# Kernel optimization log

Measured on AMD Instinct MI355X. Metric: run time of the kernel, lower is better.

Reference implementation:

```python
import jax, jax.numpy as jnp
import numpy as np

D_MODEL, D_K, D_V, H = 64, 32, 32, 8
B, HH, WW = 2, 48, 48
NQ = HH * WW


def setup_inputs() -> dict:
    key = jax.random.key(0)
    ks = jax.random.split(key, 16)
    inp = {
        "queries": jax.random.normal(ks[0], (B, D_MODEL, HH, WW), jnp.float32),
        "keys": jax.random.normal(ks[1], (B, D_MODEL, HH, WW), jnp.float32),
        "values": jax.random.normal(ks[2], (B, D_MODEL, HH, WW), jnp.float32),
        "attention_weights": jax.random.uniform(ks[3], (B, H, NQ, NQ), jnp.float32),
        "attention_mask": jax.random.randint(ks[4], (B, H, NQ, NQ), 0, 2) > 0,
        # Linear params: torch init normal(std=0.001) weights, zero bias
        "Wq": 0.001 * jax.random.normal(ks[5], (H * D_K, D_MODEL), jnp.float32),
        "bq": jnp.zeros((H * D_K,), jnp.float32),
        "Wk": 0.001 * jax.random.normal(ks[6], (H * D_K, D_MODEL), jnp.float32),
        "bk": jnp.zeros((H * D_K,), jnp.float32),
        "Wv": 0.001 * jax.random.normal(ks[7], (H * D_V, D_MODEL), jnp.float32),
        "bv": jnp.zeros((H * D_V,), jnp.float32),
        "Wo": 0.001 * jax.random.normal(ks[8], (D_MODEL, H * D_V), jnp.float32),
        "bo": jnp.zeros((D_MODEL,), jnp.float32),
    }
    return inp


def reference(queries, keys, values, attention_weights, attention_mask,
              Wq, bq, Wk, bk, Wv, bv, Wo, bo):
    b, c, hh, ww = queries.shape
    nq = hh * ww
    # torch .view(b, -1, c) on contiguous (b,c,h,w) is a raw row-major reshape
    qf = queries.reshape(b, nq, c)
    kf = keys.reshape(b, nq, c)
    vf = values.reshape(b, nq, c)
    q = (qf @ Wq.T + bq).reshape(b, nq, H, D_K).transpose(0, 2, 1, 3)  # b h nq dk
    k = (kf @ Wk.T + bk).reshape(b, nq, H, D_K).transpose(0, 2, 1, 3)  # b h nk dk
    v = (vf @ Wv.T + bv).reshape(b, nq, H, D_V).transpose(0, 2, 1, 3)  # b h nk dv
    att = jnp.einsum('bhqd,bhkd->bhqk', q, k) / np.sqrt(D_K).astype(np.float32)
    att = att * attention_weights
    att = jnp.where(attention_mask, -jnp.inf, att)
    att = jax.nn.softmax(att, axis=-1)  # dropout is identity in eval mode
    out = jnp.einsum('bhqk,bhkd->bhqd', att, v)
    out = out.transpose(0, 2, 1, 3).reshape(b, nq, H * D_V)
    out = out @ Wo.T + bo  # (b, nq, d_model)
    return out.reshape(b, -1, hh, ww)  # (b, d_model, h, w)
```

## Files before the change

kernel.cpp:

```cpp
#include <hip/hip_runtime.h>


typedef __attribute__((ext_vector_type(8))) short bf16x8;
typedef __attribute__((ext_vector_type(4))) float f32x4;

constexpr int B_  = 2;
constexpr int H_  = 8;
constexpr int NQ_ = 2304;
constexpr int DM_ = 64;
constexpr int DK_ = 32;
constexpr int NT_ = NQ_ / 32;
constexpr float SCALE_ = 0.17677669529663687f;

static __device__ __forceinline__ unsigned short f2bf(float f) {
    unsigned int u = __builtin_bit_cast(unsigned int, f);
    u += 0x7fffu + ((u >> 16) & 1u);
    return (unsigned short)(u >> 16);
}

__global__ void detect_mask_k(const unsigned int* __restrict__ m, int* __restrict__ flag) {
    int t = threadIdx.x;
    unsigned int v = 0;
    for (int k = 0; k < 16; ++k) v |= m[t * 16 + k];
    unsigned long long b = __ballot(v > 1u);
    if (t == 0) *flag = (b != 0ull) ? 1 : 0;
}

__global__ __launch_bounds__(256) void proj_qkv_k(
    const float* __restrict__ qin, const float* __restrict__ kin, const float* __restrict__ vin,
    const float* __restrict__ Wq, const float* __restrict__ bq,
    const float* __restrict__ Wk, const float* __restrict__ bk,
    const float* __restrict__ Wv, const float* __restrict__ bv,
    unsigned short* __restrict__ Qbf, unsigned short* __restrict__ Kbf,
    unsigned short* __restrict__ Vbf)
{
    const int sel = blockIdx.y;
    const float* in  = sel == 0 ? qin : (sel == 1 ? kin : vin);
    const float* W   = sel == 0 ? Wq  : (sel == 1 ? Wk  : Wv);
    const float* bia = sel == 0 ? bq  : (sel == 1 ? bk  : bv);

    const int rt = blockIdx.x;
    const int b  = rt / (NQ_ / 8);
    const int r0 = (rt % (NQ_ / 8)) * 8;

    __shared__ alignas(16) float ins[8][64];
    const int t = threadIdx.x;
    const float4* src = reinterpret_cast<const float4*>(in + ((size_t)b * NQ_ + r0) * DM_);
    if (t < 128) reinterpret_cast<float4*>(&ins[0][0])[t] = src[t];
    __syncthreads();

    float acc[8];
#pragma unroll
    for (int r = 0; r < 8; ++r) acc[r] = 0.f;
    const float* wrow = W + t * DM_;
    for (int m = 0; m < DM_; ++m) {
        float wv = wrow[m];
#pragma unroll
        for (int r = 0; r < 8; ++r) acc[r] += ins[r][m] * wv;
    }
    const float bb = bia[t];
    const int h = t >> 5, d = t & 31;
#pragma unroll
    for (int r = 0; r < 8; ++r) {
        unsigned short bvv = f2bf(acc[r] + bb);
        if (sel == 2) Vbf[(((size_t)b * H_ + h) * DK_ + d) * NQ_ + (r0 + r)] = bvv;
        else {
            unsigned short* out = (sel == 1) ? Kbf : Qbf;
            out[(((size_t)b * H_ + h) * NQ_ + (r0 + r)) * DK_ + d] = bvv;
        }
    }
}

__global__ __launch_bounds__(64) void attn_k(
    const unsigned short* __restrict__ Qbf,
    const unsigned short* __restrict__ Kbf,
    const unsigned short* __restrict__ Vbf,
    const float* __restrict__ attw,
    const unsigned char* __restrict__ maskb,
    const int* __restrict__ flagp,
    float* __restrict__ Omid)
{
    const int lane = threadIdx.x;
    const int l15 = lane & 15, hi = lane >> 4;
    const int bid = blockIdx.x;
    const int bh  = bid / (NQ_ / 16);
    const int it  = bid % (NQ_ / 16);
    const int i0  = it * 16;
    const int b   = bh / H_, h = bh % H_;
    const size_t mstride = (*flagp) ? 1 : 4;

    __shared__ alignas(16) unsigned short Plds[16][40];

    const unsigned short* qbase = Qbf + (size_t)bh * NQ_ * DK_;
    const unsigned short* kbase = Kbf + (size_t)bh * NQ_ * DK_;
    const unsigned short* vbase = Vbf + (size_t)bh * DK_ * NQ_;
    const float* wbase = attw + (size_t)bh * NQ_ * NQ_;
    const size_t mbase = (size_t)bh * NQ_ * NQ_;

    bf16x8 qa = *reinterpret_cast<const bf16x8*>(qbase + (size_t)(i0 + l15) * DK_ + 8 * hi);

    f32x4 oacc0 = {0.f, 0.f, 0.f, 0.f}, oacc1 = {0.f, 0.f, 0.f, 0.f};
    const f32x4 zero = {0.f, 0.f, 0.f, 0.f};
    float mrun[4], lrun[4];
#pragma unroll
    for (int r = 0; r < 4; ++r) { mrun[r] = -1e30f; lrun[r] = 0.f; }

    for (int t = 0; t < NT_; ++t) {
        const int j0 = t * 32;
        bf16x8 kb0 = *reinterpret_cast<const bf16x8*>(kbase + (size_t)(j0 + l15) * DK_ + 8 * hi);
        bf16x8 kb1 = *reinterpret_cast<const bf16x8*>(kbase + (size_t)(j0 + 16 + l15) * DK_ + 8 * hi);
        f32x4 s0 = __builtin_amdgcn_mfma_f32_16x16x32_bf16(qa, kb0, zero, 0, 0, 0);
        f32x4 s1 = __builtin_amdgcn_mfma_f32_16x16x32_bf16(qa, kb1, zero, 0, 0, 0);

        float x0[4], x1[4];
#pragma unroll
        for (int r = 0; r < 4; ++r) {
            const int row = i0 + 4 * hi + r;
            const size_t rb = (size_t)row * NQ_;
            float w0 = wbase[rb + j0 + l15];
            float w1 = wbase[rb + j0 + 16 + l15];
            bool k0 = maskb[(mbase + rb + j0 + l15) * mstride] != 0;
            bool k1 = maskb[(mbase + rb + j0 + 16 + l15) * mstride] != 0;
            float xv0 = s0[r] * SCALE_ * w0;
            float xv1 = s1[r] * SCALE_ * w1;
            x0[r] = k0 ? -1e30f : xv0;
            x1[r] = k1 ? -1e30f : xv1;
        }

        float p0v[4], p1v[4];
#pragma unroll
        for (int r = 0; r < 4; ++r) {
            float tm = fmaxf(x0[r], x1[r]);
#pragma unroll
            for (int sh = 1; sh < 16; sh <<= 1) tm = fmaxf(tm, __shfl_xor(tm, sh, 64));
            float mnew = fmaxf(mrun[r], tm);
            float rf = expf(mrun[r] - mnew);
            float p0 = expf(x0[r] - mnew);
            float p1 = expf(x1[r] - mnew);
            float ts = p0 + p1;
#pragma unroll
            for (int sh = 1; sh < 16; sh <<= 1) ts += __shfl_xor(ts, sh, 64);
            lrun[r] = lrun[r] * rf + ts;
            mrun[r] = mnew;
            oacc0[r] *= rf;
            oacc1[r] *= rf;
            p0v[r] = p0; p1v[r] = p1;
        }

#pragma unroll
        for (int r = 0; r < 4; ++r) {
            Plds[4 * hi + r][l15]      = f2bf(p0v[r]);
            Plds[4 * hi + r][16 + l15] = f2bf(p1v[r]);
        }
        asm volatile("s_waitcnt lgkmcnt(0)" ::: "memory");
        bf16x8 pa  = *reinterpret_cast<const bf16x8*>(&Plds[l15][8 * hi]);
        bf16x8 vb0 = *reinterpret_cast<const bf16x8*>(vbase + (size_t)(l15) * NQ_ + j0 + 8 * hi);
        bf16x8 vb1 = *reinterpret_cast<const bf16x8*>(vbase + (size_t)(16 + l15) * NQ_ + j0 + 8 * hi);
        oacc0 = __builtin_amdgcn_mfma_f32_16x16x32_bf16(pa, vb0, oacc0, 0, 0, 0);
        oacc1 = __builtin_amdgcn_mfma_f32_16x16x32_bf16(pa, vb1, oacc1, 0, 0, 0);
    }

    float* ob = Omid + (size_t)b * NQ_ * 256 + h * DK_;
#pragma unroll
    for (int r = 0; r < 4; ++r) {
        float inv = 1.0f / lrun[r];
        const int row = i0 + 4 * hi + r;
        ob[(size_t)row * 256 + l15]      = oacc0[r] * inv;
        ob[(size_t)row * 256 + 16 + l15] = oacc1[r] * inv;
    }
}

__global__ __launch_bounds__(256) void proj_out_k(
    const float* __restrict__ Omid, const float* __restrict__ Wo,
    const float* __restrict__ bo, float* __restrict__ out)
{
    const int rt = blockIdx.x;
    const int b  = rt / (NQ_ / 16);
    const int r0 = (rt % (NQ_ / 16)) * 16;

    __shared__ alignas(16) float lds[16][256];
    const int t = threadIdx.x;
    const float4* src = reinterpret_cast<const float4*>(Omid + ((size_t)b * NQ_ + r0) * 256);
#pragma unroll
    for (int k = 0; k < 4; ++k) reinterpret_cast<float4*>(&lds[0][0])[t + k * 256] = src[t + k * 256];
    __syncthreads();

    const int m = t & 63, rg = t >> 6;
    float acc[4] = {0.f, 0.f, 0.f, 0.f};
    const float* wrow = Wo + m * 256;
    for (int c = 0; c < 256; ++c) {
        float wv = wrow[c];
#pragma unroll
        for (int rr = 0; rr < 4; ++rr) acc[rr] += lds[rg * 4 + rr][c] * wv;
    }
    const float bb = bo[m];
#pragma unroll
    for (int rr = 0; rr < 4; ++rr)
        out[((size_t)b * NQ_ + r0 + rg * 4 + rr) * 64 + m] = acc[rr] + bb;
}

extern "C" void kernel_launch(void* const* d_in, const int* in_sizes, int n_in,
                              void* d_out, int out_size, void* d_ws, size_t ws_size,
                              hipStream_t stream)
{
    (void)in_sizes; (void)n_in; (void)out_size; (void)ws_size;
    const float* qin  = (const float*)d_in[0];
    const float* kin  = (const float*)d_in[1];
    const float* vin  = (const float*)d_in[2];
    const float* attw = (const float*)d_in[3];
    const void*  mask = d_in[4];
    const float* Wq = (const float*)d_in[5];
    const float* bq = (const float*)d_in[6];
    const float* Wk = (const float*)d_in[7];
    const float* bk = (const float*)d_in[8];
    const float* Wv = (const float*)d_in[9];
    const float* bv = (const float*)d_in[10];
    const float* Wo = (const float*)d_in[11];
    const float* bo = (const float*)d_in[12];

    char* ws = (char*)d_ws;
    unsigned short* Qbf = (unsigned short*)(ws);
    unsigned short* Kbf = (unsigned short*)(ws + 2359296);
    unsigned short* Vbf = (unsigned short*)(ws + 4718592);
    float*          Omid = (float*)(ws + 7077888);
    int*            flag = (int*)(ws + 11796480);

    detect_mask_k<<<1, 64, 0, stream>>>((const unsigned int*)mask, flag);
    proj_qkv_k<<<dim3(B_ * NQ_ / 8, 3), 256, 0, stream>>>(
        qin, kin, vin, Wq, bq, Wk, bk, Wv, bv, Qbf, Kbf, Vbf);
    attn_k<<<B_ * H_ * (NQ_ / 16), 64, 0, stream>>>(
        Qbf, Kbf, Vbf, attw, (const unsigned char*)mask, flag, Omid);
    proj_out_k<<<B_ * NQ_ / 16, 256, 0, stream>>>(Omid, Wo, bo, (float*)d_out);
}
```

Measured before the change: 235.1 us.

## Transpose score MFMA for vectorized weight/mask loads and split KV into chunks

The score MFMA now computes K·Q^T, so each lane owns one query row with four consecutive keys. Attention weights and mask can then be loaded as 16-byte vectors instead of scalar gathers, and P is packed straight into registers with no LDS round trip. The key dimension is split into three chunks across grid.y, which adds parallelism and waves per block, and a new combine kernel merges the partial max/sum/output. Costs are the extra kernel launch, workspace traffic for the partials, and cross-lane shuffles to rescale the accumulators.

```diff
diff --git a/kernel.cpp b/kernel.cpp
--- a/kernel.cpp
+++ b/kernel.cpp
@@ -2,7 +2,9 @@
 
 
 typedef __attribute__((ext_vector_type(8))) short bf16x8;
+typedef __attribute__((ext_vector_type(4))) short bf16x4;
 typedef __attribute__((ext_vector_type(4))) float f32x4;
+typedef __attribute__((ext_vector_type(4))) unsigned int u32x4;
 
 constexpr int B_  = 2;
 constexpr int H_  = 8;
@@ -10,7 +12,18 @@
 constexpr int DM_ = 64;
 constexpr int DK_ = 32;
 constexpr int NT_ = NQ_ / 32;
+constexpr int CH_ = 3;
+constexpr int TPC_ = NT_ / CH_;
+constexpr int GT_ = B_ * H_ * (NQ_ / 16);
 constexpr float SCALE_ = 0.17677669529663687f;
+
+constexpr size_t OFF_Q    = 0;
+constexpr size_t OFF_K    = 2359296;
+constexpr size_t OFF_V    = 4718592;
+constexpr size_t OFF_OMID = 7077888;
+constexpr size_t OFF_FLAG = 11796480;
+constexpr size_t OFF_OP   = 11796736;
+constexpr size_t OFF_ML   = 25952512;
 
 static __device__ __forceinline__ unsigned short f2bf(float f) {
     unsigned int u = __builtin_bit_cast(unsigned int, f);
@@ -71,103 +84,160 @@
     }
 }
 
-__global__ __launch_bounds__(64) void attn_k(
+__global__ __launch_bounds__(256) void attn_k(
     const unsigned short* __restrict__ Qbf,
     const unsigned short* __restrict__ Kbf,
     const unsigned short* __restrict__ Vbf,
     const float* __restrict__ attw,
     const unsigned char* __restrict__ maskb,
     const int* __restrict__ flagp,
-    float* __restrict__ Omid)
-{
-    const int lane = threadIdx.x;
+    float* __restrict__ Opart,
+    float* __restrict__ MLpart)
+{
+    const int lane = threadIdx.x & 63;
     const int l15 = lane & 15, hi = lane >> 4;
-    const int bid = blockIdx.x;
-    const int bh  = bid / (NQ_ / 16);
-    const int it  = bid % (NQ_ / 16);
-    const int i0  = it * 16;
-    const int b   = bh / H_, h = bh % H_;
-    const size_t mstride = (*flagp) ? 1 : 4;
-
-    __shared__ alignas(16) unsigned short Plds[16][40];
+    const int g = blockIdx.x * 4 + (threadIdx.x >> 6);
+    const int chunk = blockIdx.y;
+    const int bh = g / (NQ_ / 16);
+    const int it = g % (NQ_ / 16);
+    const int i0 = it * 16;
+    const bool isbyte = (*flagp) != 0;
 
     const unsigned short* qbase = Qbf + (size_t)bh * NQ_ * DK_;
     const unsigned short* kbase = Kbf + (size_t)bh * NQ_ * DK_;
     const unsigned short* vbase = Vbf + (size_t)bh * DK_ * NQ_;
-    const float* wbase = attw + (size_t)bh * NQ_ * NQ_;
-    const size_t mbase = (size_t)bh * NQ_ * NQ_;
-
-    bf16x8 qa = *reinterpret_cast<const bf16x8*>(qbase + (size_t)(i0 + l15) * DK_ + 8 * hi);
+
+    const int q = i0 + l15;
+    bf16x8 qb = *reinterpret_cast<const bf16x8*>(qbase + (size_t)q * DK_ + 8 * hi);
+
+    const float* wrow = attw + ((size_t)bh * NQ_ + q) * NQ_;
+    const size_t mrow = ((size_t)bh * NQ_ + q) * NQ_;
 
     f32x4 oacc0 = {0.f, 0.f, 0.f, 0.f}, oacc1 = {0.f, 0.f, 0.f, 0.f};
     const f32x4 zero = {0.f, 0.f, 0.f, 0.f};
-    float mrun[4], lrun[4];
-#pragma unroll
-    for (int r = 0; r < 4; ++r) { mrun[r] = -1e30f; lrun[r] = 0.f; }
-
-    for (int t = 0; t < NT_; ++t) {
+    float mrun = -1e30f, lrun = 0.f;
+
+    const int t0 = chunk * TPC_, t1 = t0 + TPC_;
+    for (int t = t0; t < t1; ++t) {
         const int j0 = t * 32;
-        bf16x8 kb0 = *reinterpret_cast<const bf16x8*>(kbase + (size_t)(j0 + l15) * DK_ + 8 * hi);
-        bf16x8 kb1 = *reinterpret_cast<const bf16x8*>(kbase + (size_t)(j0 + 16 + l15) * DK_ + 8 * hi);
-        f32x4 s0 = __builtin_amdgcn_mfma_f32_16x16x32_bf16(qa, kb0, zero, 0, 0, 0);
-        f32x4 s1 = __builtin_amdgcn_mfma_f32_16x16x32_bf16(qa, kb1, zero, 0, 0, 0);
+        bf16x8 ka0 = *reinterpret_cast<const bf16x8*>(kbase + (size_t)(j0 + l15) * DK_ + 8 * hi);
+        bf16x8 ka1 = *reinterpret_cast<const bf16x8*>(kbase + (size_t)(j0 + 16 + l15) * DK_ + 8 * hi);
+        f32x4 s0 = __builtin_amdgcn_mfma_f32_16x16x32_bf16(ka0, qb, zero, 0, 0, 0);
+        f32x4 s1 = __builtin_amdgcn_mfma_f32_16x16x32_bf16(ka1, qb, zero, 0, 0, 0);
+
+        f32x4 w0 = *reinterpret_cast<const f32x4*>(wrow + j0 + 4 * hi);
+        f32x4 w1 = *reinterpret_cast<const f32x4*>(wrow + j0 + 16 + 4 * hi);
+        unsigned int ba, bb;
+        if (isbyte) {
+            ba = *reinterpret_cast<const unsigned int*>(maskb + mrow + j0 + 4 * hi);
+            bb = *reinterpret_cast<const unsigned int*>(maskb + mrow + j0 + 16 + 4 * hi);
+        } else {
+            u32x4 A = *reinterpret_cast<const u32x4*>(maskb + (mrow + j0 + 4 * hi) * 4);
+            u32x4 Bv = *reinterpret_cast<const u32x4*>(maskb + (mrow + j0 + 16 + 4 * hi) * 4);
+            ba = (A[0] & 1u) | ((A[1] & 1u) << 8) | ((A[2] & 1u) << 16) | ((A[3] & 1u) << 24);
+            bb = (Bv[0] & 1u) | ((Bv[1] & 1u) << 8) | ((Bv[2] & 1u) << 16) | ((Bv[3] & 1u) << 24);
+        }
 
         float x0[4], x1[4];
 #pragma unroll
         for (int r = 0; r < 4; ++r) {
-            const int row = i0 + 4 * hi + r;
-            const size_t rb = (size_t)row * NQ_;
-            float w0 = wbase[rb + j0 + l15];
-            float w1 = wbase[rb + j0 + 16 + l15];
-            bool k0 = maskb[(mbase + rb + j0 + l15) * mstride] != 0;
-            bool k1 = maskb[(mbase + rb + j0 + 16 + l15) * mstride] != 0;
-            float xv0 = s0[r] * SCALE_ * w0;
-            float xv1 = s1[r] * SCALE_ * w1;
-            x0[r] = k0 ? -1e30f : xv0;
-            x1[r] = k1 ? -1e30f : xv1;
-        }
-
-        float p0v[4], p1v[4];
+            x0[r] = ((ba >> (8 * r)) & 0xffu) ? -1e30f : s0[r] * (SCALE_ * w0[r]);
+            x1[r] = ((bb >> (8 * r)) & 0xffu) ? -1e30f : s1[r] * (SCALE_ * w1[r]);
+        }
+
+        float tm = fmaxf(fmaxf(fmaxf(x0[0], x0[1]), fmaxf(x0[2], x0[3])),
+                         fmaxf(fmaxf(x1[0], x1[1]), fmaxf(x1[2], x1[3])));
+        tm = fmaxf(tm, __shfl_xor(tm, 16, 64));
+        tm = fmaxf(tm, __shfl_xor(tm, 32, 64));
+        float mnew = fmaxf(mrun, tm);
+        float rf = __expf(mrun - mnew);
+        float p0[4], p1[4], ts = 0.f;
 #pragma unroll
         for (int r = 0; r < 4; ++r) {
-            float tm = fmaxf(x0[r], x1[r]);
-#pragma unroll
-            for (int sh = 1; sh < 16; sh <<= 1) tm = fmaxf(tm, __shfl_xor(tm, sh, 64));
-            float mnew = fmaxf(mrun[r], tm);
-            float rf = expf(mrun[r] - mnew);
-            float p0 = expf(x0[r] - mnew);
-            float p1 = expf(x1[r] - mnew);
-            float ts = p0 + p1;
-#pragma unroll
-            for (int sh = 1; sh < 16; sh <<= 1) ts += __shfl_xor(ts, sh, 64);
-            lrun[r] = lrun[r] * rf + ts;
-            mrun[r] = mnew;
-            oacc0[r] *= rf;
-            oacc1[r] *= rf;
-            p0v[r] = p0; p1v[r] = p1;
-        }
+            p0[r] = __expf(x0[r] - mnew);
+            p1[r] = __expf(x1[r] - mnew);
+            ts += p0[r] + p1[r];
+        }
+        ts += __shfl_xor(ts, 16, 64);
+        ts += __shfl_xor(ts, 32, 64);
+        lrun = lrun * rf + ts;
+        mrun = mnew;
 
 #pragma unroll
         for (int r = 0; r < 4; ++r) {
-            Plds[4 * hi + r][l15]      = f2bf(p0v[r]);
-            Plds[4 * hi + r][16 + l15] = f2bf(p1v[r]);
-        }
-        asm volatile("s_waitcnt lgkmcnt(0)" ::: "memory");
-        bf16x8 pa  = *reinterpret_cast<const bf16x8*>(&Plds[l15][8 * hi]);
-        bf16x8 vb0 = *reinterpret_cast<const bf16x8*>(vbase + (size_t)(l15) * NQ_ + j0 + 8 * hi);
-        bf16x8 vb1 = *reinterpret_cast<const bf16x8*>(vbase + (size_t)(16 + l15) * NQ_ + j0 + 8 * hi);
+            float rfr = __shfl(rf, 4 * hi + r, 64);
+            oacc0[r] *= rfr;
+            oacc1[r] *= rfr;
+        }
+
+        bf16x8 pa;
+#pragma unroll
+        for (int r = 0; r < 4; ++r) {
+            pa[r]     = (short)f2bf(p0[r]);
+            pa[4 + r] = (short)f2bf(p1[r]);
+        }
+        bf16x4 v00 = *reinterpret_cast<const bf16x4*>(vbase + (size_t)l15 * NQ_ + j0 + 4 * hi);
+        bf16x4 v01 = *reinterpret_cast<const bf16x4*>(vbase + (size_t)l15 * NQ_ + j0 + 16 + 4 * hi);
+        bf16x4 v10 = *reinterpret_cast<const bf16x4*>(vbase + (size_t)(16 + l15) * NQ_ + j0 + 4 * hi);
+        bf16x4 v11 = *reinterpret_cast<const bf16x4*>(vbase + (size_t)(16 + l15) * NQ_ + j0 + 16 + 4 * hi);
+        bf16x8 vb0 = __builtin_shufflevector(v00, v01, 0, 1, 2, 3, 4, 5, 6, 7);
+        bf16x8 vb1 = __builtin_shufflevector(v10, v11, 0, 1, 2, 3, 4, 5, 6, 7);
         oacc0 = __builtin_amdgcn_mfma_f32_16x16x32_bf16(pa, vb0, oacc0, 0, 0, 0);
         oacc1 = __builtin_amdgcn_mfma_f32_16x16x32_bf16(pa, vb1, oacc1, 0, 0, 0);
     }
 
-    float* ob = Omid + (size_t)b * NQ_ * 256 + h * DK_;
+    float* op = Opart + ((size_t)chunk * GT_ + g) * 512;
 #pragma unroll
     for (int r = 0; r < 4; ++r) {
-        float inv = 1.0f / lrun[r];
-        const int row = i0 + 4 * hi + r;
-        ob[(size_t)row * 256 + l15]      = oacc0[r] * inv;
-        ob[(size_t)row * 256 + 16 + l15] = oacc1[r] * inv;
-    }
+        op[(4 * hi + r) * 32 + l15]      = oacc0[r];
+        op[(4 * hi + r) * 32 + 16 + l15] = oacc1[r];
+    }
+    if (hi == 0) {
+        float* mlp = MLpart + ((size_t)chunk * GT_ + g) * 32;
+        mlp[l15]      = mrun;
+        mlp[16 + l15] = lrun;
+    }
+}
+
+__global__ __launch_bounds__(64) void combine_k(
+    const float* __restrict__ Opart, const float* __restrict__ MLpart,
+    float* __restrict__ Omid)
+{
+    const int g = blockIdx.x;
+    const int lane = threadIdx.x;
+    const int row = lane >> 2;
+    const int c4  = (lane & 3) * 8;
+    const int bh = g / (NQ_ / 16);
+    const int it = g % (NQ_ / 16);
+    const int b = bh / H_, h = bh % H_;
+
+    float m[CH_], l[CH_];
+#pragma unroll
+    for (int c = 0; c < CH_; ++c) {
+        const float* mlp = MLpart + ((size_t)c * GT_ + g) * 32;
+        m[c] = mlp[row];
+        l[c] = mlp[16 + row];
+    }
+    float mg = fmaxf(fmaxf(m[0], m[1]), m[2]);
+    float e0 = __expf(m[0] - mg), e1 = __expf(m[1] - mg), e2 = __expf(m[2] - mg);
+    float lg = l[0] * e0 + l[1] * e1 + l[2] * e2;
+    float inv = 1.0f / lg;
+
+    const size_t ob = (size_t)row * 32 + c4;
+    f32x4 a0 = {0.f,0.f,0.f,0.f}, a1 = {0.f,0.f,0.f,0.f};
+    float ee[CH_] = {e0, e1, e2};
+#pragma unroll
+    for (int c = 0; c < CH_; ++c) {
+        const float* opp = Opart + ((size_t)c * GT_ + g) * 512 + ob;
+        f32x4 t0 = *reinterpret_cast<const f32x4*>(opp);
+        f32x4 t1 = *reinterpret_cast<const f32x4*>(opp + 4);
+        a0 += t0 * ee[c];
+        a1 += t1 * ee[c];
+    }
+    a0 *= inv; a1 *= inv;
+    float* dst = Omid + ((size_t)b * NQ_ + it * 16 + row) * 256 + h * 32 + c4;
+    *reinterpret_cast<f32x4*>(dst)     = a0;
+    *reinterpret_cast<f32x4*>(dst + 4) = a1;
 }
 
 __global__ __launch_bounds__(256) void proj_out_k(
@@ -219,16 +289,19 @@
     const float* bo = (const float*)d_in[12];
 
     char* ws = (char*)d_ws;
-    unsigned short* Qbf = (unsigned short*)(ws);
-    unsigned short* Kbf = (unsigned short*)(ws + 2359296);
-    unsigned short* Vbf = (unsigned short*)(ws + 4718592);
-    float*          Omid = (float*)(ws + 7077888);
-    int*            flag = (int*)(ws + 11796480);
+    unsigned short* Qbf   = (unsigned short*)(ws + OFF_Q);
+    unsigned short* Kbf   = (unsigned short*)(ws + OFF_K);
+    unsigned short* Vbf   = (unsigned short*)(ws + OFF_V);
+    float*          Omid  = (float*)(ws + OFF_OMID);
+    int*            flag  = (int*)(ws + OFF_FLAG);
+    float*          Opart = (float*)(ws + OFF_OP);
+    float*          MLp   = (float*)(ws + OFF_ML);
 
     detect_mask_k<<<1, 64, 0, stream>>>((const unsigned int*)mask, flag);
     proj_qkv_k<<<dim3(B_ * NQ_ / 8, 3), 256, 0, stream>>>(
         qin, kin, vin, Wq, bq, Wk, bk, Wv, bv, Qbf, Kbf, Vbf);
-    attn_k<<<B_ * H_ * (NQ_ / 16), 64, 0, stream>>>(
-        Qbf, Kbf, Vbf, attw, (const unsigned char*)mask, flag, Omid);
+    attn_k<<<dim3(GT_ / 4, CH_), 256, 0, stream>>>(
+        Qbf, Kbf, Vbf, attw, (const unsigned char*)mask, flag, Opart, MLp);
+    combine_k<<<GT_, 64, 0, stream>>>(Opart, MLp, Omid);
     proj_out_k<<<B_ * NQ_ / 16, 256, 0, stream>>>(Omid, Wo, bo, (float*)d_out);
 }
```

Result: slower. 260.8 us (+10.9%).
